# Optimization experiments

Hardware: AMD Instinct MI355X
Metric: run time of the kernel (lower is better)

The kernel has to match this reference:

```python
import jax, jax.numpy as jnp
import numpy as np

B, L, H, N, COND = 32, 32768, 32, 16, 4
N2 = N // 2  # S4D stores N/2 complex conjugate-pair modes


def setup_inputs() -> dict:
    key = jax.random.key(0)
    ks = jax.random.split(key, 8)
    x = jax.random.normal(ks[0], (B, L, H), jnp.float32)
    cond = jax.random.normal(ks[1], (B, COND), jnp.float32)
    # S4D kernel parameters (state-spaces minimal S4D init)
    log_dt = np.log(1e-3) + jax.random.uniform(ks[2], (H,), jnp.float32) * (np.log(1e-1) - np.log(1e-3))
    C_re = jax.random.normal(ks[3], (H, N2), jnp.float32) * (0.5 ** 0.5)
    C_im = jax.random.normal(ks[4], (H, N2), jnp.float32) * (0.5 ** 0.5)
    log_A_real = jnp.log(0.5 * jnp.ones((H, N2), jnp.float32))
    A_imag = jnp.pi * jnp.tile(jnp.arange(N2, dtype=jnp.float32), (H, 1))
    D = jax.random.normal(ks[5], (H,), jnp.float32)
    # FiLM linear: cond -> (gamma, beta)
    film_W = jax.random.normal(ks[6], (COND, 2 * H), jnp.float32) / np.sqrt(COND)
    film_b = jnp.zeros((2 * H,), jnp.float32)
    return dict(x=x, cond=cond, log_dt=log_dt, C_re=C_re, C_im=C_im,
                log_A_real=log_A_real, A_imag=A_imag, D=D,
                film_W=film_W, film_b=film_b)


def reference(x, cond, log_dt, C_re, C_im, log_A_real, A_imag, D, film_W, film_b):
    # x: (B, L, H) -> DSSM over channel-major layout (B, H, L)
    u = jnp.transpose(x, (0, 2, 1))  # B H L
    # --- S4D kernel: K[h, l] = 2 * Re( sum_n C~_hn * exp(dt_h * A_hn * l) )
    dt = jnp.exp(log_dt)[:, None]                      # (H, 1)
    A = -jnp.exp(log_A_real) + 1j * A_imag             # (H, N2) complex
    dtA = A * dt                                       # (H, N2)
    Ct = (C_re + 1j * C_im) * (jnp.exp(dtA) - 1.0) / A # discretized C
    vand = jnp.exp(dtA[:, :, None] * jnp.arange(L, dtype=jnp.float32))  # (H, N2, L)
    K = 2.0 * jnp.einsum('hn,hnl->hl', Ct, vand).real  # (H, L)
    # --- causal convolution via FFT on length-2L circular pad
    n_fft = 2 * L
    y = jnp.fft.irfft(jnp.fft.rfft(u, n=n_fft) * jnp.fft.rfft(K, n=n_fft), n=n_fft)[..., :L]
    y = y + u * D[:, None]                             # skip connection
    y = jnp.transpose(y, (0, 2, 1))                    # back to (B, L, H)
    # --- FiLM conditioning
    gb = cond @ film_W + film_b                        # (B, 2H)
    gamma, beta = gb[:, :H], gb[:, H:]
    y = gamma[:, None, :] * y + beta[:, None, :]
    # --- activation
    return jax.nn.gelu(y)
```

## Files before the change

kernel.cpp:

```cpp
#include <hip/hip_runtime.h>

typedef float v2f __attribute__((ext_vector_type(2)));

#define BB 32
#define LL 32768
#define HH 32
#define NN2 8
#define NCOND 4
#define NCHUNK 256
#define LC (LL / NCHUNK)

#define PARAM_OFF 0
#define WLC_OFF   1024
#define FILM_OFF  1536
#define S_OFF     4096
#define SZ_S      (BB * HH * NCHUNK * 16)

static __device__ __forceinline__ v2f vfma(v2f a, v2f b, v2f c) {
  return __builtin_elementwise_fma(a, b, c);
}

__global__ void setup_kernel(const float* __restrict__ log_dt,
                             const float* __restrict__ C_re,
                             const float* __restrict__ C_im,
                             const float* __restrict__ log_A_real,
                             const float* __restrict__ A_imag,
                             const float* __restrict__ cond,
                             const float* __restrict__ film_W,
                             const float* __restrict__ film_b,
                             float* __restrict__ ws) {
  int idx = blockIdx.x * blockDim.x + threadIdx.x;
  if (idx < HH * NN2) {
    int h = idx >> 3, n = idx & (NN2 - 1);
    float dt = expf(log_dt[h]);
    float ar = -expf(log_A_real[idx]);
    float ai = A_imag[idx];
    float dr = ar * dt, di = ai * dt;
    float er = expf(dr);
    float wr = er * cosf(di);
    float wi = er * sinf(di);
    float den = ar * ar + ai * ai;
    float tr = ((wr - 1.f) * ar + wi * ai) / den;
    float ti = (wi * ar - (wr - 1.f) * ai) / den;
    float cr = C_re[idx], ci = C_im[idx];
    float ctr = 2.f * (cr * tr - ci * ti);
    float cti = 2.f * (cr * ti + ci * tr);
    float* p = ws + PARAM_OFF + h * 32;
    p[n] = wr; p[n + 8] = wi; p[n + 16] = ctr; p[n + 24] = cti;
    float eL  = expf(dr * (float)LC);
    float wlr = eL * cosf(di * (float)LC);
    float wli = eL * sinf(di * (float)LC);
    float* q = ws + WLC_OFF + idx * 2;
    q[0] = wlr; q[1] = wli;
  }
  int f = idx - HH * NN2;
  if (f >= 0 && f < BB * HH) {
    int b = f >> 5, h = f & (HH - 1);
    float g  = film_b[h];
    float be = film_b[h + HH];
    #pragma unroll
    for (int c2 = 0; c2 < NCOND; c2++) {
      float cv = cond[b * NCOND + c2];
      g  = fmaf(cv, film_W[c2 * 2 * HH + h], g);
      be = fmaf(cv, film_W[c2 * 2 * HH + HH + h], be);
    }
    float* p = ws + FILM_OFF + f * 2;
    p[0] = g; p[1] = be;
  }
}

__global__ __launch_bounds__(256) void pass_a(const float* __restrict__ x,
                                              float* __restrict__ ws) {
  const int flat = blockIdx.x * 256 + threadIdx.x;
  const int h = flat & (HH - 1);
  const int c = (flat >> 5) & (NCHUNK - 1);
  const int b = flat >> 13;
  const v2f* pp = (const v2f*)(ws + PARAM_OFF + h * 32);
  v2f wr[4], wi[4], zr[4], zi[4];
  #pragma unroll
  for (int g = 0; g < 4; g++) {
    wr[g] = pp[g]; wi[g] = pp[4 + g];
    zr[g] = (v2f){0.f, 0.f}; zi[g] = (v2f){0.f, 0.f};
  }
  const float* xp = x + ((size_t)b * LL + (size_t)c * LC) * HH + h;
  for (int i = 0; i < LC; i += 8) {
    float u[8];
    #pragma unroll
    for (int j = 0; j < 8; j++) u[j] = xp[(size_t)(i + j) * HH];
    #pragma unroll
    for (int j = 0; j < 8; j++) {
      v2f us = (v2f){u[j], u[j]};
      #pragma unroll
      for (int g = 0; g < 4; g++) {
        v2f t0  = vfma(-wi[g], zi[g], us);
        v2f nzr = vfma(wr[g], zr[g], t0);
        v2f nzi = vfma(wr[g], zi[g], wi[g] * zr[g]);
        zr[g] = nzr; zi[g] = nzi;
      }
    }
  }
  v2f* Sp = (v2f*)(ws + S_OFF + (size_t)flat * 16);
  #pragma unroll
  for (int g = 0; g < 4; g++) { Sp[g] = zr[g]; Sp[4 + g] = zi[g]; }
}

__global__ void pass_b(float* __restrict__ ws) {
  int idx = blockIdx.x * blockDim.x + threadIdx.x;
  int n = idx & (NN2 - 1);
  int h = (idx >> 3) & (HH - 1);
  int b = idx >> 8;
  float wlr = ws[WLC_OFF + (h * NN2 + n) * 2];
  float wli = ws[WLC_OFF + (h * NN2 + n) * 2 + 1];
  float Zr = 0.f, Zi = 0.f;
  const size_t stride = (size_t)HH * 16;
  size_t base = ((size_t)b * NCHUNK * HH + h) * 16 + n;
  for (int c = 0; c < NCHUNK; c++) {
    float* pr = ws + S_OFF + base + (size_t)c * stride;
    float sr = pr[0];
    float si = pr[8];
    pr[0] = Zr;
    pr[8] = Zi;
    float nZr = fmaf(wlr, Zr, fmaf(-wli, Zi, sr));
    float nZi = fmaf(wlr, Zi, fmaf(wli, Zr, si));
    Zr = nZr; Zi = nZi;
  }
}

__global__ __launch_bounds__(256) void pass_c(const float* __restrict__ x,
                                              const float* __restrict__ Dv,
                                              float* __restrict__ out,
                                              float* __restrict__ ws) {
  const int flat = blockIdx.x * 256 + threadIdx.x;
  const int h = flat & (HH - 1);
  const int c = (flat >> 5) & (NCHUNK - 1);
  const int b = flat >> 13;
  const v2f* pp = (const v2f*)(ws + PARAM_OFF + h * 32);
  v2f wr[4], wi[4], ctr[4], cti[4], zr[4], zi[4];
  #pragma unroll
  for (int g = 0; g < 4; g++) {
    wr[g] = pp[g]; wi[g] = pp[4 + g]; ctr[g] = pp[8 + g]; cti[g] = pp[12 + g];
  }
  const v2f* Zp = (const v2f*)(ws + S_OFF + (size_t)flat * 16);
  #pragma unroll
  for (int g = 0; g < 4; g++) { zr[g] = Zp[g]; zi[g] = Zp[4 + g]; }
  float gamma = ws[FILM_OFF + ((size_t)b * HH + h) * 2];
  float beta  = ws[FILM_OFF + ((size_t)b * HH + h) * 2 + 1];
  float dcoef = Dv[h];
  const size_t off = ((size_t)b * LL + (size_t)c * LC) * HH + h;
  const float* xp = x + off;
  float* op = out + off;
  for (int i = 0; i < LC; i += 8) {
    float u[8];
    #pragma unroll
    for (int j = 0; j < 8; j++) u[j] = xp[(size_t)(i + j) * HH];
    #pragma unroll
    for (int j = 0; j < 8; j++) {
      v2f us = (v2f){u[j], u[j]};
      v2f acc = (v2f){0.f, 0.f};
      #pragma unroll
      for (int g = 0; g < 4; g++) {
        v2f t0  = vfma(-wi[g], zi[g], us);
        v2f nzr = vfma(wr[g], zr[g], t0);
        v2f nzi = vfma(wr[g], zi[g], wi[g] * zr[g]);
        zr[g] = nzr; zi[g] = nzi;
        acc = vfma(ctr[g], nzr, acc);
        acc = vfma(-cti[g], nzi, acc);
      }
      float y = acc.x + acc.y;
      y = fmaf(dcoef, u[j], y);
      y = fmaf(gamma, y, beta);
      float y3   = y * y * y;
      float targ = 0.7978845608f * fmaf(0.044715f, y3, y);
      float e    = __expf(2.f * targ);
      float th   = 1.f - __fdividef(2.f, e + 1.f);
      op[(size_t)(i + j) * HH] = 0.5f * y * (1.f + th);
    }
  }
}

extern "C" void kernel_launch(void* const* d_in, const int* in_sizes, int n_in,
                              void* d_out, int out_size, void* d_ws, size_t ws_size,
                              hipStream_t stream) {
  const float* x          = (const float*)d_in[0];
  const float* cond       = (const float*)d_in[1];
  const float* log_dt     = (const float*)d_in[2];
  const float* C_re       = (const float*)d_in[3];
  const float* C_im       = (const float*)d_in[4];
  const float* log_A_real = (const float*)d_in[5];
  const float* A_imag     = (const float*)d_in[6];
  const float* Dv         = (const float*)d_in[7];
  const float* film_W     = (const float*)d_in[8];
  const float* film_b     = (const float*)d_in[9];
  float* out = (float*)d_out;
  float* ws  = (float*)d_ws;

  setup_kernel<<<5, 256, 0, stream>>>(log_dt, C_re, C_im, log_A_real, A_imag,
                                      cond, film_W, film_b, ws);
  pass_a<<<(BB * HH * NCHUNK) / 256, 256, 0, stream>>>(x, ws);
  pass_b<<<(BB * HH * NN2) / 256, 256, 0, stream>>>(ws);
  pass_c<<<(BB * HH * NCHUNK) / 256, 256, 0, stream>>>(x, Dv, out, ws);
}
```

Before: 317.2 us.

## Replace serial chunk-carry scan with parallel Hillis-Steele scan in shared memory

The pass_b kernel previously walked all 256 chunk states serially, one thread per (b,h,n), with 32 blocks doing strided global reads and writes. It now runs one block per (b,h) with one thread per chunk and performs a log-step Hillis-Steele scan in LDS, squaring the chunk-transition multiplier at each step. Each thread then writes the exclusive prefix back. The output store in pass_c also becomes nontemporal to avoid polluting cache. The scan does more total work, adds block barriers and changes the floating-point summation order.

Result: faster. 307.3 us (-3.1%).

```diff
diff --git a/kernel.cpp b/kernel.cpp
--- a/kernel.cpp
+++ b/kernel.cpp
@@ -104,25 +104,72 @@
   for (int g = 0; g < 4; g++) { Sp[g] = zr[g]; Sp[4 + g] = zi[g]; }
 }
 
-__global__ void pass_b(float* __restrict__ ws) {
-  int idx = blockIdx.x * blockDim.x + threadIdx.x;
-  int n = idx & (NN2 - 1);
-  int h = (idx >> 3) & (HH - 1);
-  int b = idx >> 8;
-  float wlr = ws[WLC_OFF + (h * NN2 + n) * 2];
-  float wli = ws[WLC_OFF + (h * NN2 + n) * 2 + 1];
-  float Zr = 0.f, Zi = 0.f;
-  const size_t stride = (size_t)HH * 16;
-  size_t base = ((size_t)b * NCHUNK * HH + h) * 16 + n;
-  for (int c = 0; c < NCHUNK; c++) {
-    float* pr = ws + S_OFF + base + (size_t)c * stride;
-    float sr = pr[0];
-    float si = pr[8];
-    pr[0] = Zr;
-    pr[8] = Zi;
-    float nZr = fmaf(wlr, Zr, fmaf(-wli, Zi, sr));
-    float nZi = fmaf(wlr, Zi, fmaf(wli, Zr, si));
-    Zr = nZr; Zi = nZi;
+__global__ __launch_bounds__(256) void pass_b(float* __restrict__ ws) {
+  const int bh = blockIdx.x;
+  const int b  = bh >> 5;
+  const int h  = bh & (HH - 1);
+  const int t  = threadIdx.x;
+
+  __shared__ __align__(16) float Lbuf[NCHUNK][18];
+
+  float* Sp = ws + S_OFF +
+              ((size_t)b * (NCHUNK * HH) + (size_t)t * HH + h) * 16;
+
+  v2f zr[4], zi[4];
+  #pragma unroll
+  for (int g = 0; g < 4; g++) {
+    zr[g] = ((const v2f*)Sp)[g];
+    zi[g] = ((const v2f*)Sp)[4 + g];
+  }
+
+  const float* q = ws + WLC_OFF + h * NN2 * 2;
+  v2f mr[4], mi[4];
+  #pragma unroll
+  for (int g = 0; g < 4; g++) {
+    mr[g] = (v2f){q[4 * g + 0], q[4 * g + 2]};
+    mi[g] = (v2f){q[4 * g + 1], q[4 * g + 3]};
+  }
+
+  v2f* rowv = (v2f*)&Lbuf[t][0];
+  #pragma unroll
+  for (int g = 0; g < 4; g++) { rowv[g] = zr[g]; rowv[4 + g] = zi[g]; }
+  __syncthreads();
+
+  #pragma unroll
+  for (int d = 1; d < NCHUNK; d <<= 1) {
+    v2f ar[4], ai[4];
+    #pragma unroll
+    for (int g = 0; g < 4; g++) { ar[g] = (v2f){0.f, 0.f}; ai[g] = (v2f){0.f, 0.f}; }
+    if (t >= d) {
+      const v2f* prow = (const v2f*)&Lbuf[t - d][0];
+      #pragma unroll
+      for (int g = 0; g < 4; g++) { ar[g] = prow[g]; ai[g] = prow[4 + g]; }
+    }
+    __syncthreads();
+    #pragma unroll
+    for (int g = 0; g < 4; g++) {
+      zr[g] = vfma(mr[g], ar[g], vfma(-mi[g], ai[g], zr[g]));
+      zi[g] = vfma(mr[g], ai[g], vfma(mi[g], ar[g], zi[g]));
+      rowv[g] = zr[g]; rowv[4 + g] = zi[g];
+      v2f nmr = vfma(mr[g], mr[g], -(mi[g] * mi[g]));
+      v2f nmi = (mr[g] + mr[g]) * mi[g];
+      mr[g] = nmr; mi[g] = nmi;
+    }
+    __syncthreads();
+  }
+
+  v2f er[4], ei[4];
+  #pragma unroll
+  for (int g = 0; g < 4; g++) { er[g] = (v2f){0.f, 0.f}; ei[g] = (v2f){0.f, 0.f}; }
+  if (t > 0) {
+    const v2f* prow = (const v2f*)&Lbuf[t - 1][0];
+    #pragma unroll
+    for (int g = 0; g < 4; g++) { er[g] = prow[g]; ei[g] = prow[4 + g]; }
+  }
+  #pragma unroll
+  for (int g = 0; g < 4; g++) {
+    ((v2f*)Sp)[g] = er[g];
+    ((v2f*)Sp)[4 + g] = ei[g];
   }
 }
 
@@ -173,7 +220,8 @@
       float targ = 0.7978845608f * fmaf(0.044715f, y3, y);
       float e    = __expf(2.f * targ);
       float th   = 1.f - __fdividef(2.f, e + 1.f);
-      op[(size_t)(i + j) * HH] = 0.5f * y * (1.f + th);
+      __builtin_nontemporal_store(0.5f * y * (1.f + th),
+                                  op + (size_t)(i + j) * HH);
     }
   }
 }
@@ -197,6 +245,6 @@
   setup_kernel<<<5, 256, 0, stream>>>(log_dt, C_re, C_im, log_A_real, A_imag,
                                       cond, film_W, film_b, ws);
   pass_a<<<(BB * HH * NCHUNK) / 256, 256, 0, stream>>>(x, ws);
-  pass_b<<<(BB * HH * NN2) / 256, 256, 0, stream>>>(ws);
+  pass_b<<<BB * HH, 256, 0, stream>>>(ws);
   pass_c<<<(BB * HH * NCHUNK) / 256, 256, 0, stream>>>(x, Dv, out, ws);
 }
```
